# Performance work log

Measured on AMD Instinct MI355X. Metric: run time of the kernel, lower is better.

Reference implementation:

```python
import jax, jax.numpy as jnp
import numpy as np

B, S, H = 1, 2048, 2048
NH, NKV, HD = 16, 4, 128          # heads, kv heads, head_dim
RHD = 64                          # rope head dim
QC, KVC = 1536, 512               # q / kv latent dims
EPS = 1e-6
SCALE = (HD + RHD) ** -0.5


def rms_norm(x, w):
    var = jnp.mean(x.astype(jnp.float32) ** 2, axis=-1, keepdims=True)
    return (x * jax.lax.rsqrt(var + EPS) * w).astype(x.dtype)


def rotate_half(x):
    x1, x2 = x[..., : x.shape[-1] // 2], x[..., x.shape[-1] // 2:]
    return jnp.concatenate([-x2, x1], axis=-1)


def apply_rope(q, k, cos, sin):
    cos = cos[:, None, :, :]  # [B,1,S,RHD]
    sin = sin[:, None, :, :]
    return q * cos + rotate_half(q) * sin, k * cos + rotate_half(k) * sin


def setup_inputs() -> dict:
    key = jax.random.key(0)
    ks = jax.random.split(key, 12)
    X = jax.random.normal(ks[0], (B, S, H), jnp.float32)
    # rotary tables
    inv_freq = 1.0 / (10000.0 ** (np.arange(0, RHD, 2, dtype=np.float32) / RHD))
    t = np.arange(S, dtype=np.float32)
    freqs = np.outer(t, inv_freq)               # [S, RHD/2]
    emb = np.concatenate([freqs, freqs], -1)    # [S, RHD]
    cos = jnp.asarray(np.cos(emb))[None].repeat(B, 0)
    sin = jnp.asarray(np.sin(emb))[None].repeat(B, 0)
    mask = jnp.tril(jnp.ones((S, S), jnp.int32))[None].repeat(B, 0)  # causal
    sc = lambda fan_in: 1.0 / np.sqrt(fan_in)
    return dict(
        X=X, cos=cos, sin=sin, mask=mask,
        w_down_q=jax.random.normal(ks[1], (H, QC), jnp.float32) * sc(H),
        w_up_q=jax.random.normal(ks[2], (QC, H), jnp.float32) * sc(QC),
        w_qr=jax.random.normal(ks[3], (QC, NH * RHD), jnp.float32) * sc(QC),
        w_down_kv=jax.random.normal(ks[4], (H, KVC), jnp.float32) * sc(H),
        w_up_k=jax.random.normal(ks[5], (KVC, NKV * HD), jnp.float32) * sc(KVC),
        w_up_v=jax.random.normal(ks[6], (KVC, NKV * HD), jnp.float32) * sc(KVC),
        w_kr=jax.random.normal(ks[7], (H, RHD), jnp.float32) * sc(H),
        w_o=jax.random.normal(ks[8], (H, H), jnp.float32) * sc(H),
        q_norm_w=jnp.ones((QC,), jnp.float32),
        k_norm_w=jnp.ones((KVC,), jnp.float32),
    )


def reference(X, cos, sin, mask, w_down_q, w_up_q, w_qr, w_down_kv,
              w_up_k, w_up_v, w_kr, w_o, q_norm_w, k_norm_w):
    bsz, q_len, _ = X.shape
    n_rep = NH // NKV
    # --- Q path: down-project, RMSNorm, up-project + rope branch ---
    cq = rms_norm(X @ w_down_q, q_norm_w)                    # [B,S,QC]
    qc = (cq @ w_up_q).reshape(bsz, q_len, NH, HD).transpose(0, 2, 1, 3)
    qr = (cq @ w_qr).reshape(bsz, q_len, NH, RHD).transpose(0, 2, 1, 3)
    # --- KV path ---
    ckv = rms_norm(X @ w_down_kv, k_norm_w)                  # [B,S,KVC]
    kc = (ckv @ w_up_k).reshape(bsz, q_len, NKV, HD).transpose(0, 2, 1, 3)
    kr = (X @ w_kr).reshape(bsz, q_len, 1, RHD).transpose(0, 2, 1, 3)
    kc = jnp.repeat(kc, n_rep, axis=1)                       # [B,NH,S,HD]
    kr = jnp.broadcast_to(kr, (bsz, NH, q_len, RHD))         # repeat_kv(kr, NH)
    qr, kr = apply_rope(qr, kr, cos, sin)
    query = jnp.concatenate([qc, qr], axis=-1)               # [B,NH,S,HD+RHD]
    key = jnp.concatenate([kc, kr], axis=-1)
    value = (ckv @ w_up_v).reshape(bsz, q_len, NKV, HD).transpose(0, 2, 1, 3)
    value = jnp.repeat(value, n_rep, axis=1)                 # [B,NH,S,HD]
    # --- attention ---
    scores = jnp.einsum('bhqd,bhkd->bhqk', query, key) * SCALE
    scores = jnp.where(mask[:, None] == 0, -1e9, scores)
    attn = jax.nn.softmax(scores, axis=-1)                   # dropout p=0
    ctx = jnp.einsum('bhqk,bhkd->bhqd', attn, value)
    ctx = ctx.transpose(0, 2, 1, 3).reshape(bsz, q_len, NH * HD)
    return ctx @ w_o, attn
```

## Files before the change

### kernel.cpp

```cpp
#include <hip/hip_runtime.h>
#include <stdint.h>

typedef __bf16 bf16;
typedef __bf16 bf16x8 __attribute__((ext_vector_type(8)));
typedef __bf16 bf16x4 __attribute__((ext_vector_type(4)));
typedef float f32x4 __attribute__((ext_vector_type(4)));

#define DEVFN static __device__ __forceinline__

constexpr int S = 2048, Hdim = 2048, NH = 16, NKV = 4, HD = 128, RHD = 64, QC = 1536, KVC = 512;
constexpr int QKD = HD + RHD;
constexpr int DN = 2112;
constexpr float RMS_EPS = 1e-6f;
constexpr float ATT_SCALE = 0.07216878364870323f;

DEVFN float wave_sum(float v) {
#pragma unroll
  for (int o = 32; o > 0; o >>= 1) v += __shfl_xor(v, o, 64);
  return v;
}
DEVFN float block_sum(float v) {
  __shared__ float red_s[4];
  v = wave_sum(v);
  int lane = threadIdx.x & 63, wid = threadIdx.x >> 6;
  if (lane == 0) red_s[wid] = v;
  __syncthreads();
  v = red_s[0] + red_s[1] + red_s[2] + red_s[3];
  __syncthreads();
  return v;
}

DEVFN void lgkm_barrier() {
  asm volatile("s_waitcnt lgkmcnt(0)" ::: "memory");
  __builtin_amdgcn_s_barrier();
}

template <typename OT>
DEVFN void gemm_core_pipe(const bf16* __restrict__ A, const bf16* __restrict__ Bt,
                          OT* __restrict__ C, int N, int lda, int ldb, int ldc,
                          int m0, int n0, float scale, int kend) {
  __shared__ alignas(16) bf16 As[2][128 * 32];
  __shared__ alignas(16) bf16 Bs[2][128 * 32];
  const int t = threadIdx.x;
  const int lane = t & 63;
  const int wm = ((t >> 7) & 1) * 64;
  const int wn = ((t >> 6) & 1) * 64;
  const int lr = lane & 15;
  const int lk = (lane >> 4) * 8;
  const int srow = t >> 2;
  const int scol = (t & 3) * 8;
  const bf16* A0 = A + (size_t)(m0 + srow) * lda + scol;
  const bf16* A1 = A + (size_t)(m0 + 64 + srow) * lda + scol;
  const bf16* B0 = Bt + (size_t)(n0 + srow) * ldb + scol;
  const bf16* B1 = Bt + (size_t)(n0 + 64 + srow) * ldb + scol;

  f32x4 acc[4][4];
#pragma unroll
  for (int i = 0; i < 4; i++)
#pragma unroll
    for (int j = 0; j < 4; j++) { f32x4 z = {0.f, 0.f, 0.f, 0.f}; acc[i][j] = z; }

  bf16x8 ca0 = *reinterpret_cast<const bf16x8*>(A0);
  bf16x8 ca1 = *reinterpret_cast<const bf16x8*>(A1);
  bf16x8 cb0 = *reinterpret_cast<const bf16x8*>(B0);
  bf16x8 cb1 = *reinterpret_cast<const bf16x8*>(B1);
  int cur = 0;
  for (int kk = 0; kk < kend; kk += 32) {
    bf16x8 na0, na1, nb0, nb1;
    if (kk + 32 < kend) {
      na0 = *reinterpret_cast<const bf16x8*>(A0 + kk + 32);
      na1 = *reinterpret_cast<const bf16x8*>(A1 + kk + 32);
      nb0 = *reinterpret_cast<const bf16x8*>(B0 + kk + 32);
      nb1 = *reinterpret_cast<const bf16x8*>(B1 + kk + 32);
    }
    *reinterpret_cast<bf16x8*>(&As[cur][t * 8]) = ca0;
    *reinterpret_cast<bf16x8*>(&As[cur][t * 8 + 2048]) = ca1;
    *reinterpret_cast<bf16x8*>(&Bs[cur][t * 8]) = cb0;
    *reinterpret_cast<bf16x8*>(&Bs[cur][t * 8 + 2048]) = cb1;
    lgkm_barrier();
    bf16x8 a[4], b[4];
#pragma unroll
    for (int i = 0; i < 4; i++)
      a[i] = *reinterpret_cast<const bf16x8*>(&As[cur][(wm + i * 16 + lr) * 32 + lk]);
#pragma unroll
    for (int i = 0; i < 4; i++)
      b[i] = *reinterpret_cast<const bf16x8*>(&Bs[cur][(wn + i * 16 + lr) * 32 + lk]);
    __builtin_amdgcn_s_setprio(1);
#pragma unroll
    for (int i = 0; i < 4; i++)
#pragma unroll
      for (int j = 0; j < 4; j++)
        acc[i][j] = __builtin_amdgcn_mfma_f32_16x16x32_bf16(a[i], b[j], acc[i][j], 0, 0, 0);
    __builtin_amdgcn_s_setprio(0);
    ca0 = na0; ca1 = na1; cb0 = nb0; cb1 = nb1;
    cur ^= 1;
  }
  const int orow = (lane >> 4) * 4;
#pragma unroll
  for (int i = 0; i < 4; i++) {
#pragma unroll
    for (int j = 0; j < 4; j++) {
      int col = n0 + wn + j * 16 + lr;
      if (col < N) {
#pragma unroll
        for (int q = 0; q < 4; q++) {
          int row = m0 + wm + i * 16 + orow + q;
          C[(size_t)row * ldc + col] = (OT)(acc[i][j][q] * scale);
        }
      }
    }
  }
}

template <typename OT>
__global__ __launch_bounds__(256) void gemm_nt(const bf16* __restrict__ A, const bf16* __restrict__ Bt,
                                               OT* __restrict__ C, int N, int K, int lda,
                                               int ldb, int ldc, float scale) {
  gemm_core_pipe<OT>(A, Bt, C, N, lda, ldb, ldc, blockIdx.y * 128, blockIdx.x * 128, scale, K);
}

__global__ __launch_bounds__(256) void gemm_up_both(const bf16* __restrict__ cqb,
                                                    const bf16* __restrict__ ckvb,
                                                    const bf16* __restrict__ wt_up1,
                                                    const bf16* __restrict__ wt_up2,
                                                    bf16* __restrict__ up1,
                                                    bf16* __restrict__ up2) {
  int id = blockIdx.x;
  if (id < 384) {
    gemm_core_pipe<bf16>(cqb, wt_up1, up1, 3072, QC, QC, 3072, (id / 24) * 128, (id % 24) * 128, 1.f, QC);
  } else {
    id -= 384;
    gemm_core_pipe<bf16>(ckvb, wt_up2, up2, 1024, KVC, KVC, 1024, (id / 8) * 128, (id % 8) * 128, 1.f, KVC);
  }
}

__global__ __launch_bounds__(512) void fa_fused(const bf16* __restrict__ qpack,
                                                const bf16* __restrict__ kpack,
                                                const bf16* __restrict__ vt,
                                                float* __restrict__ attn,
                                                bf16* __restrict__ ctxb) {
  const int h = blockIdx.y;
  const int g = h >> 2;
  __shared__ alignas(16) bf16 Ks[2][64 * 200];
  __shared__ alignas(16) bf16 Vs[3][128 * 72];
  __shared__ alignas(16) bf16 Ps[3][64 * 72];
  float2* sb = reinterpret_cast<float2*>(&Vs[0][0]);
  float2* statf = sb + 128;

  const int t = threadIdx.x;
  const int lane = t & 63;
  const int w = t >> 6;
  const int wm = (w & 3) * 16;
  const int kh = w >> 2;
  const int lr = lane & 15;
  const int hi = lane >> 4;
  const int lk = hi * 8;
  const int kr0 = t / 24, kc0 = (t % 24) * 8;
  const int kr1 = (t + 512) / 24, kc1 = ((t + 512) % 24) * 8;
  const int kr2 = (t + 1024) / 24, kc2 = ((t + 1024) % 24) * 8;
  const int vr0 = t >> 3, vc0 = (t & 7) * 8;
  const int vr1 = (t + 512) >> 3, vc1 = ((t + 512) & 7) * 8;

  const bf16* Qg = qpack + (size_t)h * S * QKD;
  const bf16* Kg = kpack + (size_t)g * S * QKD;
  const bf16* Vg = vt + (size_t)g * HD * S;
  float* Ah = attn + (size_t)h * S * S;
  bf16* C = ctxb + h * HD;

  for (int sub = 0; sub < 2; ++sub) {
    const int m0 = sub ? (1984 - 64 * blockIdx.x) : (64 * blockIdx.x);
    const int ntiles = sub ? (32 - blockIdx.x) : (blockIdx.x + 1);
    const int kend = m0 + 64;
    __syncthreads();

    bf16x8 qf[6];
#pragma unroll
    for (int ks = 0; ks < 6; ++ks)
      qf[ks] = *reinterpret_cast<const bf16x8*>(&Qg[(size_t)(m0 + wm + lr) * QKD + ks * 32 + lk]);

    float mreg[4] = {-1e30f, -1e30f, -1e30f, -1e30f};
    float lreg[4] = {0.f, 0.f, 0.f, 0.f};
    bf16x8 ck0 = *reinterpret_cast<const bf16x8*>(&Kg[(size_t)kr0 * QKD + kc0]);
    bf16x8 ck1 = *reinterpret_cast<const bf16x8*>(&Kg[(size_t)kr1 * QKD + kc1]);
    bf16x8 ck2 = *reinterpret_cast<const bf16x8*>(&Kg[(size_t)kr2 * QKD + kc2]);
    int cur = 0;
    for (int ti = 0; ti < ntiles; ++ti) {
      const int kt = ti * 64;
      bf16x8 nk0, nk1, nk2;
      if (ti + 1 < ntiles) {
        nk0 = *reinterpret_cast<const bf16x8*>(&Kg[(size_t)(kt + 64 + kr0) * QKD + kc0]);
        nk1 = *reinterpret_cast<const bf16x8*>(&Kg[(size_t)(kt + 64 + kr1) * QKD + kc1]);
        nk2 = *reinterpret_cast<const bf16x8*>(&Kg[(size_t)(kt + 64 + kr2) * QKD + kc2]);
      }
      *reinterpret_cast<bf16x8*>(&Ks[cur][kr0 * 200 + kc0]) = ck0;
      *reinterpret_cast<bf16x8*>(&Ks[cur][kr1 * 200 + kc1]) = ck1;
      *reinterpret_cast<bf16x8*>(&Ks[cur][kr2 * 200 + kc2]) = ck2;
      lgkm_barrier();
      f32x4 acc[2];
#pragma unroll
      for (int kb = 0; kb < 2; kb++) { f32x4 z = {0.f, 0.f, 0.f, 0.f}; acc[kb] = z; }
      __builtin_amdgcn_s_setprio(1);
#pragma unroll
      for (int ks = 0; ks < 6; ++ks) {
#pragma unroll
        for (int kb = 0; kb < 2; ++kb) {
          bf16x8 b = *reinterpret_cast<const bf16x8*>(&Ks[cur][(kh * 32 + kb * 16 + lr) * 200 + ks * 32 + lk]);
          acc[kb] = __builtin_amdgcn_mfma_f32_16x16x32_bf16(qf[ks], b, acc[kb], 0, 0, 0);
        }
      }
      __builtin_amdgcn_s_setprio(0);
      const int colb = kt + kh * 32 + lr;
#pragma unroll
      for (int q = 0; q < 4; ++q) {
        const int rowg = m0 + wm + hi * 4 + q;
        bool u0 = (colb <= rowg), u1 = (colb + 16 <= rowg);
        float s0 = u0 ? acc[0][q] * ATT_SCALE : -1e30f;
        float s1 = u1 ? acc[1][q] * ATT_SCALE : -1e30f;
        float nm = fmaxf(mreg[q], fmaxf(s0, s1));
        float e0 = u0 ? __expf(s0 - nm) : 0.f;
        float e1 = u1 ? __expf(s1 - nm) : 0.f;
        lreg[q] = lreg[q] * __expf(mreg[q] - nm) + e0 + e1;
        mreg[q] = nm;
      }
      ck0 = nk0; ck1 = nk1; ck2 = nk2;
      cur ^= 1;
    }
#pragma unroll
    for (int q = 0; q < 4; ++q) {
      float m = mreg[q], l = lreg[q];
#pragma unroll
      for (int o = 1; o < 16; o <<= 1) {
        float mo = __shfl_xor(m, o, 64);
        float lo = __shfl_xor(l, o, 64);
        float M = fmaxf(m, mo);
        l = l * __expf(m - M) + lo * __expf(mo - M);
        m = M;
      }
      mreg[q] = m; lreg[q] = l;
    }
    __syncthreads();
    if (lr == 0) {
#pragma unroll
      for (int q = 0; q < 4; ++q)
        sb[kh * 64 + wm + hi * 4 + q] = make_float2(mreg[q], lreg[q]);
    }
    __syncthreads();
    if (w < 4 && lr == 0) {
#pragma unroll
      for (int q = 0; q < 4; ++q) {
        int r = wm + hi * 4 + q;
        float2 a = sb[r], b = sb[64 + r];
        float M = fmaxf(a.x, b.x);
        float L = a.y * __expf(a.x - M) + b.y * __expf(b.x - M);
        statf[r] = make_float2(M, 1.0f / L);
      }
    }
    __syncthreads();
    float mr[4], invl[4];
#pragma unroll
    for (int q = 0; q < 4; ++q) {
      float2 sv = statf[wm + hi * 4 + q];
      mr[q] = sv.x; invl[q] = sv.y;
    }
    __syncthreads();

    f32x4 accp[4];
#pragma unroll
    for (int j = 0; j < 4; j++) { f32x4 z = {0.f, 0.f, 0.f, 0.f}; accp[j] = z; }
    ck0 = *reinterpret_cast<const bf16x8*>(&Kg[(size_t)kr0 * QKD + kc0]);
    ck1 = *reinterpret_cast<const bf16x8*>(&Kg[(size_t)kr1 * QKD + kc1]);
    ck2 = *reinterpret_cast<const bf16x8*>(&Kg[(size_t)kr2 * QKD + kc2]);
    bf16x8 cv0 = *reinterpret_cast<const bf16x8*>(&Vg[(size_t)vr0 * S + vc0]);
    bf16x8 cv1 = *reinterpret_cast<const bf16x8*>(&Vg[(size_t)vr1 * S + vc1]);
    cur = 0;
    int pb = 0;
    for (int ti = 0; ti < ntiles; ++ti) {
      const int kt = ti * 64;
      bf16x8 nk0, nk1, nk2, nv0, nv1;
      if (ti + 1 < ntiles) {
        nk0 = *reinterpret_cast<const bf16x8*>(&Kg[(size_t)(kt + 64 + kr0) * QKD + kc0]);
        nk1 = *reinterpret_cast<const bf16x8*>(&Kg[(size_t)(kt + 64 + kr1) * QKD + kc1]);
        nk2 = *reinterpret_cast<const bf16x8*>(&Kg[(size_t)(kt + 64 + kr2) * QKD + kc2]);
        nv0 = *reinterpret_cast<const bf16x8*>(&Vg[(size_t)vr0 * S + kt + 64 + vc0]);
        nv1 = *reinterpret_cast<const bf16x8*>(&Vg[(size_t)vr1 * S + kt + 64 + vc1]);
      }
      *reinterpret_cast<bf16x8*>(&Ks[cur][kr0 * 200 + kc0]) = ck0;
      *reinterpret_cast<bf16x8*>(&Ks[cur][kr1 * 200 + kc1]) = ck1;
      *reinterpret_cast<bf16x8*>(&Ks[cur][kr2 * 200 + kc2]) = ck2;
      *reinterpret_cast<bf16x8*>(&Vs[pb][vr0 * 72 + vc0]) = cv0;
      *reinterpret_cast<bf16x8*>(&Vs[pb][vr1 * 72 + vc1]) = cv1;
      lgkm_barrier();
      f32x4 acc[2];
#pragma unroll
      for (int kb = 0; kb < 2; kb++) { f32x4 z = {0.f, 0.f, 0.f, 0.f}; acc[kb] = z; }
      __builtin_amdgcn_s_setprio(1);
#pragma unroll
      for (int ks = 0; ks < 6; ++ks) {
#pragma unroll
        for (int kb = 0; kb < 2; ++kb) {
          bf16x8 b = *reinterpret_cast<const bf16x8*>(&Ks[cur][(kh * 32 + kb * 16 + lr) * 200 + ks * 32 + lk]);
          acc[kb] = __builtin_amdgcn_mfma_f32_16x16x32_bf16(qf[ks], b, acc[kb], 0, 0, 0);
        }
      }
      __builtin_amdgcn_s_setprio(0);
      const int colb = kt + kh * 32 + lr;
#pragma unroll
      for (int kb = 0; kb < 2; ++kb) {
#pragma unroll
        for (int q = 0; q < 4; ++q) {
          const int rloc = wm + hi * 4 + q;
          const int rowg = m0 + rloc;
          const int col = colb + kb * 16;
          float s = acc[kb][q] * ATT_SCALE;
          float p = (col <= rowg) ? __expf(s - mr[q]) * invl[q] : 0.f;
          Ah[(size_t)rowg * S + col] = p;
          Ps[pb][rloc * 72 + kh * 32 + kb * 16 + lr] = (bf16)p;
        }
      }
      if (ti > 0) {
        const int pp = (pb == 0) ? 2 : pb - 1;
        __builtin_amdgcn_s_setprio(1);
#pragma unroll
        for (int ks = 0; ks < 2; ++ks) {
          bf16x8 a = *reinterpret_cast<const bf16x8*>(&Ps[pp][(wm + lr) * 72 + ks * 32 + lk]);
#pragma unroll
          for (int j = 0; j < 4; ++j) {
            bf16x8 b = *reinterpret_cast<const bf16x8*>(&Vs[pp][(kh * 64 + j * 16 + lr) * 72 + ks * 32 + lk]);
            accp[j] = __builtin_amdgcn_mfma_f32_16x16x32_bf16(a, b, accp[j], 0, 0, 0);
          }
        }
        __builtin_amdgcn_s_setprio(0);
      }
      ck0 = nk0; ck1 = nk1; ck2 = nk2; cv0 = nv0; cv1 = nv1;
      cur ^= 1;
      pb = (pb == 2) ? 0 : pb + 1;
    }
    lgkm_barrier();
    {
      const int pp = (pb == 0) ? 2 : pb - 1;
#pragma unroll
      for (int ks = 0; ks < 2; ++ks) {
        bf16x8 a = *reinterpret_cast<const bf16x8*>(&Ps[pp][(wm + lr) * 72 + ks * 32 + lk]);
#pragma unroll
        for (int j = 0; j < 4; ++j) {
          bf16x8 b = *reinterpret_cast<const bf16x8*>(&Vs[pp][(kh * 64 + j * 16 + lr) * 72 + ks * 32 + lk]);
          accp[j] = __builtin_amdgcn_mfma_f32_16x16x32_bf16(a, b, accp[j], 0, 0, 0);
        }
      }
    }

    const float4 zz = make_float4(0.f, 0.f, 0.f, 0.f);
    {
      const int zr = t >> 3, zc0 = (t & 7) * 4;
      float* zrow = Ah + (size_t)(m0 + zr) * S;
      for (int k = kend + zc0; k < S; k += 32) *reinterpret_cast<float4*>(zrow + k) = zz;
    }

#pragma unroll
    for (int j = 0; j < 4; ++j) {
      const int d = kh * 64 + j * 16 + lr;
#pragma unroll
      for (int q = 0; q < 4; ++q) {
        const int rowg = m0 + wm + hi * 4 + q;
        C[(size_t)rowg * Hdim + d] = (bf16)accp[j][q];
      }
    }
  }
}

struct TJobs {
  const float* src[8];
  bf16* dst[8];
  int R[8], C[8], tiles[8];
};

__global__ __launch_bounds__(256) void prep(const float* __restrict__ Xf,
                                            bf16* __restrict__ Xb, TJobs J) {
  const int t = threadIdx.x;
  int id = blockIdx.x;
  if (id < 2048) {
    size_t i = (size_t)id * 256 + t;
    float4 f0 = *reinterpret_cast<const float4*>(Xf + i * 8);
    float4 f1 = *reinterpret_cast<const float4*>(Xf + i * 8 + 4);
    bf16x8 v;
    v[0] = (bf16)f0.x; v[1] = (bf16)f0.y; v[2] = (bf16)f0.z; v[3] = (bf16)f0.w;
    v[4] = (bf16)f1.x; v[5] = (bf16)f1.y; v[6] = (bf16)f1.z; v[7] = (bf16)f1.w;
    *reinterpret_cast<bf16x8*>(Xb + i * 8) = v;
    return;
  }
  int tile = id - 2048;
  int j = 0;
  while (tile >= J.tiles[j]) { tile -= J.tiles[j]; ++j; }
  const int C = J.C[j], R = J.R[j];
  int tcn = C >> 5;
  int rb = (tile / tcn) * 32, cb = (tile % tcn) * 32;
  const float* in = J.src[j];
  bf16* out = J.dst[j];
  __shared__ float tl[32][33];
  int tx = t & 31, ty = t >> 5;
#pragma unroll
  for (int q = 0; q < 32; q += 8)
    tl[ty + q][tx] = in[(size_t)(rb + ty + q) * C + cb + tx];
  __syncthreads();
#pragma unroll
  for (int q = 0; q < 32; q += 8)
    out[(size_t)(cb + ty + q) * R + rb + tx] = (bf16)tl[tx][ty + q];
}

__global__ __launch_bounds__(256) void rmsnorm_fused(const float* __restrict__ dproj,
                                                     const float* __restrict__ qw,
                                                     const float* __restrict__ kw,
                                                     bf16* __restrict__ cqb,
                                                     bf16* __restrict__ ckvb) {
  int row = blockIdx.x;
  bool isq = (blockIdx.y == 0);
  int C = isq ? QC : KVC;
  const float* p = dproj + (size_t)row * DN + (isq ? 0 : QC);
  const float* w = isq ? qw : kw;
  bf16* out = (isq ? cqb : ckvb) + (size_t)row * C;
  float ss = 0.f;
  for (int i = threadIdx.x * 4; i < C; i += 1024) {
    float4 v = *reinterpret_cast<const float4*>(p + i);
    ss += v.x * v.x + v.y * v.y + v.z * v.z + v.w * v.w;
  }
  ss = block_sum(ss);
  float r = rsqrtf(ss / (float)C + RMS_EPS);
  for (int i = threadIdx.x * 4; i < C; i += 1024) {
    float4 v = *reinterpret_cast<const float4*>(p + i);
    float4 g = *reinterpret_cast<const float4*>(w + i);
    bf16x4 o;
    o[0] = (bf16)(v.x * r * g.x); o[1] = (bf16)(v.y * r * g.y);
    o[2] = (bf16)(v.z * r * g.z); o[3] = (bf16)(v.w * r * g.w);
    *reinterpret_cast<bf16x4*>(out + i) = o;
  }
}

__global__ __launch_bounds__(256) void pack_all(const bf16* __restrict__ up1,
                                                const bf16* __restrict__ up2,
                                                const float* __restrict__ dproj,
                                                const float* __restrict__ cosp,
                                                const float* __restrict__ sinp,
                                                bf16* __restrict__ qpack,
                                                bf16* __restrict__ kpack,
                                                bf16* __restrict__ vt) {
  const int t = threadIdx.x;
  int id = blockIdx.x;
  if (id < 3072) {
    int idx = id * 256 + t;
    const int P = NH * S * 16;
    if (idx < P) {
      int d8 = idx & 15, s = (idx >> 4) & (S - 1), h = idx >> 15;
      int4 v = *reinterpret_cast<const int4*>(up1 + (size_t)s * 3072 + h * HD + d8 * 8);
      *reinterpret_cast<int4*>(qpack + ((size_t)h * S + s) * QKD + d8 * 8) = v;
    } else {
      int j = idx - P;
      int d0 = (j & 7) * 8, s = (j >> 3) & (S - 1), h = j >> 14;
      const bf16* xr = up1 + (size_t)s * 3072 + 2048 + h * RHD;
      bf16x8 xa = *reinterpret_cast<const bf16x8*>(xr + d0);
      bf16x8 xb = *reinterpret_cast<const bf16x8*>(xr + (d0 ^ 32));
      float sign = (d0 < 32) ? -1.f : 1.f;
      const float* cr = cosp + s * RHD + d0;
      const float* sr = sinp + s * RHD + d0;
      bf16x8 o;
#pragma unroll
      for (int i = 0; i < 8; i++)
        o[i] = (bf16)((float)xa[i] * cr[i] + sign * (float)xb[i] * sr[i]);
      *reinterpret_cast<bf16x8*>(qpack + ((size_t)h * S + s) * QKD + HD + d0) = o;
    }
    return;
  }
  if (id < 3648) {
    int idx = (id - 3072) * 256 + t;
    const int P = NKV * S * 16;
    if (idx < P) {
      int d8 = idx & 15, s = (idx >> 4) & (S - 1), g = idx >> 15;
      int4 v = *reinterpret_cast<const int4*>(up2 + (size_t)s * 1024 + g * HD + d8 * 8);
      *reinterpret_cast<int4*>(kpack + ((size_t)g * S + s) * QKD + d8 * 8) = v;
    } else {
      int j = idx - P;
      int d0 = (j & 7) * 8, s = j >> 3;
      const float* xr = dproj + (size_t)s * DN + 2048;
      float4 a0 = *reinterpret_cast<const float4*>(xr + d0);
      float4 a1 = *reinterpret_cast<const float4*>(xr + d0 + 4);
      float4 b0 = *reinterpret_cast<const float4*>(xr + (d0 ^ 32));
      float4 b1 = *reinterpret_cast<const float4*>(xr + (d0 ^ 32) + 4);
      float sign = (d0 < 32) ? -1.f : 1.f;
      const float* cr = cosp + s * RHD + d0;
      const float* sr = sinp + s * RHD + d0;
      float xa[8] = {a0.x, a0.y, a0.z, a0.w, a1.x, a1.y, a1.z, a1.w};
      float xb[8] = {b0.x, b0.y, b0.z, b0.w, b1.x, b1.y, b1.z, b1.w};
      bf16x8 o;
#pragma unroll
      for (int i = 0; i < 8; i++)
        o[i] = (bf16)(xa[i] * cr[i] + sign * xb[i] * sr[i]);
#pragma unroll
      for (int g = 0; g < NKV; g++)
        *reinterpret_cast<bf16x8*>(kpack + ((size_t)g * S + s) * QKD + HD + d0) = o;
    }
    return;
  }
  int tile = id - 3648;
  int cb = (tile & 15) * 32;
  int rb = (tile >> 4) * 32;
  __shared__ float tl[32][33];
  int tx = t & 31, ty = t >> 5;
  const bf16* in = up2 + 512;
#pragma unroll
  for (int q = 0; q < 32; q += 8)
    tl[ty + q][tx] = (float)in[(size_t)(rb + ty + q) * 1024 + cb + tx];
  __syncthreads();
#pragma unroll
  for (int q = 0; q < 32; q += 8)
    vt[(size_t)(cb + ty + q) * S + rb + tx] = (bf16)tl[tx][ty + q];
}

extern "C" void kernel_launch(void* const* d_in, const int* in_sizes, int n_in, void* d_out,
                              int out_size, void* d_ws, size_t ws_size, hipStream_t stream) {
  const float* Xf = (const float*)d_in[0];
  const float* cosp = (const float*)d_in[1];
  const float* sinp = (const float*)d_in[2];
  const float* w_down_q = (const float*)d_in[4];
  const float* w_up_q = (const float*)d_in[5];
  const float* w_qr = (const float*)d_in[6];
  const float* w_down_kv = (const float*)d_in[7];
  const float* w_up_k = (const float*)d_in[8];
  const float* w_up_v = (const float*)d_in[9];
  const float* w_kr = (const float*)d_in[10];
  const float* w_o = (const float*)d_in[11];
  const float* q_norm_w = (const float*)d_in[12];
  const float* k_norm_w = (const float*)d_in[13];

  float* out0 = (float*)d_out;
  float* attn = out0 + (size_t)S * Hdim;

  char* base = (char*)d_ws;
  size_t off = 0;
  auto carve = [&](size_t bytes) -> void* {
    void* p = base + off;
    off += (bytes + 255) & ~(size_t)255;
    return p;
  };
  bf16* Xb      = (bf16*)carve((size_t)S * Hdim * 2);
  bf16* wt_down = (bf16*)carve((size_t)2176 * 2048 * 2);
  bf16* wt_up1  = (bf16*)carve((size_t)3072 * QC * 2);
  bf16* wt_up2  = (bf16*)carve((size_t)1024 * KVC * 2);
  bf16* wt_o    = (bf16*)carve((size_t)Hdim * Hdim * 2);
  float* dproj  = (float*)carve((size_t)S * DN * 4);
  bf16* cqb     = (bf16*)carve((size_t)S * QC * 2);
  bf16* ckvb    = (bf16*)carve((size_t)S * KVC * 2);
  bf16* up1     = (bf16*)carve((size_t)S * 3072 * 2);
  bf16* up2     = (bf16*)carve((size_t)S * 1024 * 2);
  bf16* qpack   = (bf16*)carve((size_t)NH * S * QKD * 2);
  bf16* kpack   = (bf16*)carve((size_t)NKV * S * QKD * 2);
  bf16* vt      = (bf16*)carve((size_t)NKV * HD * S * 2);
  bf16* ctxb    = (bf16*)carve((size_t)S * Hdim * 2);
  (void)in_sizes; (void)n_in; (void)out_size; (void)ws_size;

  TJobs J;
  const float* srcs[8] = {w_down_q, w_down_kv, w_kr, w_up_q, w_qr, w_up_k, w_up_v, w_o};
  bf16* dsts[8] = {wt_down, wt_down + (size_t)QC * 2048, wt_down + (size_t)2048 * 2048,
                   wt_up1, wt_up1 + (size_t)2048 * QC, wt_up2, wt_up2 + (size_t)512 * KVC, wt_o};
  int Rs[8] = {2048, 2048, 2048, 1536, 1536, 512, 512, 2048};
  int Cs[8] = {1536, 512, 64, 2048, 1024, 512, 512, 2048};
  int total_tiles = 0;
  for (int j = 0; j < 8; j++) {
    J.src[j] = srcs[j]; J.dst[j] = dsts[j]; J.R[j] = Rs[j]; J.C[j] = Cs[j];
    J.tiles[j] = (Rs[j] / 32) * (Cs[j] / 32);
    total_tiles += J.tiles[j];
  }

  prep<<<2048 + total_tiles, 256, 0, stream>>>(Xf, Xb, J);
  gemm_nt<float><<<dim3(17, 16), 256, 0, stream>>>(Xb, wt_down, dproj, DN, Hdim, Hdim, Hdim, DN, 1.f);
  rmsnorm_fused<<<dim3(S, 2), 256, 0, stream>>>(dproj, q_norm_w, k_norm_w, cqb, ckvb);
  gemm_up_both<<<512, 256, 0, stream>>>(cqb, ckvb, wt_up1, wt_up2, up1, up2);
  pack_all<<<4672, 256, 0, stream>>>(up1, up2, dproj, cosp, sinp, qpack, kpack, vt);
  fa_fused<<<dim3(16, NH), 512, 0, stream>>>(qpack, kpack, vt, attn, ctxb);
  gemm_nt<float><<<dim3(16, 16), 256, 0, stream>>>(ctxb, wt_o, out0, Hdim, Hdim, Hdim, Hdim, Hdim, 1.f);
}
```

Baseline: 306.8 us.

## Split fused attention into stats and PV kernels with key-range halves

The fused attention kernel becomes two kernels, each launched with twice the blocks: every block handles one half of the key tiles. The first kernel writes partial row max and sum statistics to global memory. The second merges the two halves' statistics, writes the probabilities, and accumulates partial context in fp32 over 32-wide key tiles. A third kernel adds the two partial contexts and converts the sum to bf16. The aim is more parallelism and occupancy than the previous 256-block grid, at the cost of extra launches, fp32 partial-context traffic, and a second read of Q and K.

Result: slower. 346.5 us (+12.9%).

```diff
diff --git a/kernel.cpp b/kernel.cpp
--- a/kernel.cpp
+++ b/kernel.cpp
@@ -134,18 +134,13 @@
   }
 }
 
-__global__ __launch_bounds__(512) void fa_fused(const bf16* __restrict__ qpack,
-                                                const bf16* __restrict__ kpack,
-                                                const bf16* __restrict__ vt,
-                                                float* __restrict__ attn,
-                                                bf16* __restrict__ ctxb) {
-  const int h = blockIdx.y;
+__global__ __launch_bounds__(512, 4) void fa_stats(const bf16* __restrict__ qpack,
+                                                   const bf16* __restrict__ kpack,
+                                                   float* __restrict__ stats2) {
+  const int ib = blockIdx.x, half = blockIdx.y, h = blockIdx.z;
   const int g = h >> 2;
   __shared__ alignas(16) bf16 Ks[2][64 * 200];
-  __shared__ alignas(16) bf16 Vs[3][128 * 72];
-  __shared__ alignas(16) bf16 Ps[3][64 * 72];
-  float2* sb = reinterpret_cast<float2*>(&Vs[0][0]);
-  float2* statf = sb + 128;
+  __shared__ float2 sb[128];
 
   const int t = threadIdx.x;
   const int lane = t & 63;
@@ -158,19 +153,15 @@
   const int kr0 = t / 24, kc0 = (t % 24) * 8;
   const int kr1 = (t + 512) / 24, kc1 = ((t + 512) % 24) * 8;
   const int kr2 = (t + 1024) / 24, kc2 = ((t + 1024) % 24) * 8;
-  const int vr0 = t >> 3, vc0 = (t & 7) * 8;
-  const int vr1 = (t + 512) >> 3, vc1 = ((t + 512) & 7) * 8;
-
   const bf16* Qg = qpack + (size_t)h * S * QKD;
   const bf16* Kg = kpack + (size_t)g * S * QKD;
-  const bf16* Vg = vt + (size_t)g * HD * S;
-  float* Ah = attn + (size_t)h * S * S;
-  bf16* C = ctxb + h * HD;
 
   for (int sub = 0; sub < 2; ++sub) {
-    const int m0 = sub ? (1984 - 64 * blockIdx.x) : (64 * blockIdx.x);
-    const int ntiles = sub ? (32 - blockIdx.x) : (blockIdx.x + 1);
-    const int kend = m0 + 64;
+    const int m0 = sub ? (1984 - 64 * ib) : (64 * ib);
+    const int ntF = sub ? (32 - ib) : (ib + 1);
+    const int n0 = (ntF + 1) >> 1;
+    const int t0 = half ? n0 : 0;
+    const int t1 = half ? ntF : n0;
     __syncthreads();
 
     bf16x8 qf[6];
@@ -180,50 +171,52 @@
 
     float mreg[4] = {-1e30f, -1e30f, -1e30f, -1e30f};
     float lreg[4] = {0.f, 0.f, 0.f, 0.f};
-    bf16x8 ck0 = *reinterpret_cast<const bf16x8*>(&Kg[(size_t)kr0 * QKD + kc0]);
-    bf16x8 ck1 = *reinterpret_cast<const bf16x8*>(&Kg[(size_t)kr1 * QKD + kc1]);
-    bf16x8 ck2 = *reinterpret_cast<const bf16x8*>(&Kg[(size_t)kr2 * QKD + kc2]);
-    int cur = 0;
-    for (int ti = 0; ti < ntiles; ++ti) {
-      const int kt = ti * 64;
-      bf16x8 nk0, nk1, nk2;
-      if (ti + 1 < ntiles) {
-        nk0 = *reinterpret_cast<const bf16x8*>(&Kg[(size_t)(kt + 64 + kr0) * QKD + kc0]);
-        nk1 = *reinterpret_cast<const bf16x8*>(&Kg[(size_t)(kt + 64 + kr1) * QKD + kc1]);
-        nk2 = *reinterpret_cast<const bf16x8*>(&Kg[(size_t)(kt + 64 + kr2) * QKD + kc2]);
-      }
-      *reinterpret_cast<bf16x8*>(&Ks[cur][kr0 * 200 + kc0]) = ck0;
-      *reinterpret_cast<bf16x8*>(&Ks[cur][kr1 * 200 + kc1]) = ck1;
-      *reinterpret_cast<bf16x8*>(&Ks[cur][kr2 * 200 + kc2]) = ck2;
-      lgkm_barrier();
-      f32x4 acc[2];
-#pragma unroll
-      for (int kb = 0; kb < 2; kb++) { f32x4 z = {0.f, 0.f, 0.f, 0.f}; acc[kb] = z; }
-      __builtin_amdgcn_s_setprio(1);
-#pragma unroll
-      for (int ks = 0; ks < 6; ++ks) {
-#pragma unroll
-        for (int kb = 0; kb < 2; ++kb) {
-          bf16x8 b = *reinterpret_cast<const bf16x8*>(&Ks[cur][(kh * 32 + kb * 16 + lr) * 200 + ks * 32 + lk]);
-          acc[kb] = __builtin_amdgcn_mfma_f32_16x16x32_bf16(qf[ks], b, acc[kb], 0, 0, 0);
+    if (t0 < t1) {
+      bf16x8 ck0 = *reinterpret_cast<const bf16x8*>(&Kg[(size_t)(t0 * 64 + kr0) * QKD + kc0]);
+      bf16x8 ck1 = *reinterpret_cast<const bf16x8*>(&Kg[(size_t)(t0 * 64 + kr1) * QKD + kc1]);
+      bf16x8 ck2 = *reinterpret_cast<const bf16x8*>(&Kg[(size_t)(t0 * 64 + kr2) * QKD + kc2]);
+      int cur = 0;
+      for (int ti = t0; ti < t1; ++ti) {
+        const int kt = ti * 64;
+        bf16x8 nk0, nk1, nk2;
+        if (ti + 1 < t1) {
+          nk0 = *reinterpret_cast<const bf16x8*>(&Kg[(size_t)(kt + 64 + kr0) * QKD + kc0]);
+          nk1 = *reinterpret_cast<const bf16x8*>(&Kg[(size_t)(kt + 64 + kr1) * QKD + kc1]);
+          nk2 = *reinterpret_cast<const bf16x8*>(&Kg[(size_t)(kt + 64 + kr2) * QKD + kc2]);
         }
-      }
-      __builtin_amdgcn_s_setprio(0);
-      const int colb = kt + kh * 32 + lr;
-#pragma unroll
-      for (int q = 0; q < 4; ++q) {
-        const int rowg = m0 + wm + hi * 4 + q;
-        bool u0 = (colb <= rowg), u1 = (colb + 16 <= rowg);
-        float s0 = u0 ? acc[0][q] * ATT_SCALE : -1e30f;
-        float s1 = u1 ? acc[1][q] * ATT_SCALE : -1e30f;
-        float nm = fmaxf(mreg[q], fmaxf(s0, s1));
-        float e0 = u0 ? __expf(s0 - nm) : 0.f;
-        float e1 = u1 ? __expf(s1 - nm) : 0.f;
-        lreg[q] = lreg[q] * __expf(mreg[q] - nm) + e0 + e1;
-        mreg[q] = nm;
-      }
-      ck0 = nk0; ck1 = nk1; ck2 = nk2;
-      cur ^= 1;
+        *reinterpret_cast<bf16x8*>(&Ks[cur][kr0 * 200 + kc0]) = ck0;
+        *reinterpret_cast<bf16x8*>(&Ks[cur][kr1 * 200 + kc1]) = ck1;
+        *reinterpret_cast<bf16x8*>(&Ks[cur][kr2 * 200 + kc2]) = ck2;
+        lgkm_barrier();
+        f32x4 acc[2];
+#pragma unroll
+        for (int kb = 0; kb < 2; kb++) { f32x4 z = {0.f, 0.f, 0.f, 0.f}; acc[kb] = z; }
+        __builtin_amdgcn_s_setprio(1);
+#pragma unroll
+        for (int ks = 0; ks < 6; ++ks) {
+#pragma unroll
+          for (int kb = 0; kb < 2; ++kb) {
+            bf16x8 b = *reinterpret_cast<const bf16x8*>(&Ks[cur][(kh * 32 + kb * 16 + lr) * 200 + ks * 32 + lk]);
+            acc[kb] = __builtin_amdgcn_mfma_f32_16x16x32_bf16(qf[ks], b, acc[kb], 0, 0, 0);
+          }
+        }
+        __builtin_amdgcn_s_setprio(0);
+        const int colb = kt + kh * 32 + lr;
+#pragma unroll
+        for (int q = 0; q < 4; ++q) {
+          const int rowg = m0 + wm + hi * 4 + q;
+          bool u0 = (colb <= rowg), u1 = (colb + 16 <= rowg);
+          float s0 = u0 ? acc[0][q] * ATT_SCALE : -1e30f;
+          float s1 = u1 ? acc[1][q] * ATT_SCALE : -1e30f;
+          float nm = fmaxf(mreg[q], fmaxf(s0, s1));
+          float e0 = u0 ? __expf(s0 - nm) : 0.f;
+          float e1 = u1 ? __expf(s1 - nm) : 0.f;
+          lreg[q] = lreg[q] * __expf(mreg[q] - nm) + e0 + e1;
+          mreg[q] = nm;
+        }
+        ck0 = nk0; ck1 = nk1; ck2 = nk2;
+        cur ^= 1;
+      }
     }
 #pragma unroll
     for (int q = 0; q < 4; ++q) {
@@ -252,105 +245,135 @@
         float2 a = sb[r], b = sb[64 + r];
         float M = fmaxf(a.x, b.x);
         float L = a.y * __expf(a.x - M) + b.y * __expf(b.x - M);
-        statf[r] = make_float2(M, 1.0f / L);
-      }
-    }
+        stats2[(((size_t)half * NH + h) * S + m0 + r) * 2] = M;
+        stats2[(((size_t)half * NH + h) * S + m0 + r) * 2 + 1] = L;
+      }
+    }
+  }
+}
+
+__global__ __launch_bounds__(512, 4) void fa_pv(const bf16* __restrict__ qpack,
+                                                const bf16* __restrict__ kpack,
+                                                const bf16* __restrict__ vt,
+                                                const float* __restrict__ stats2,
+                                                float* __restrict__ attn,
+                                                float* __restrict__ octxA,
+                                                float* __restrict__ octxB) {
+  const int ib = blockIdx.x, half = blockIdx.y, h = blockIdx.z;
+  const int g = h >> 2;
+  __shared__ alignas(16) bf16 Ks[2][32 * 200];
+  __shared__ alignas(16) bf16 Vs[3][128 * 40];
+  __shared__ alignas(16) bf16 Ps[3][64 * 40];
+
+  const int t = threadIdx.x;
+  const int lane = t & 63;
+  const int w = t >> 6;
+  const int wm = (w & 3) * 16;
+  const int kh = w >> 2;
+  const int lr = lane & 15;
+  const int hi = lane >> 4;
+  const int lk = hi * 8;
+  const int kr0 = t / 24, kc0 = (t % 24) * 8;
+  const int kr1 = (t + 512) / 24, kc1 = ((t + 512) % 24) * 8;
+  const int vr0 = t >> 2, vc0 = (t & 3) * 8;
+
+  const bf16* Qg = qpack + (size_t)h * S * QKD;
+  const bf16* Kg = kpack + (size_t)g * S * QKD;
+  const bf16* Vg = vt + (size_t)g * HD * S;
+  float* Ah = attn + (size_t)h * S * S;
+  float* octx = half ? octxB : octxA;
+
+  for (int sub = 0; sub < 2; ++sub) {
+    const int m0 = sub ? (1984 - 64 * ib) : (64 * ib);
+    const int ntF = sub ? (64 - 2 * ib) : (2 * ib + 2);
+    const int nh = ntF >> 1;
+    const int t0 = half * nh, t1 = t0 + nh;
+    const int kend = m0 + 64;
     __syncthreads();
+
+    bf16x8 qf[6];
+#pragma unroll
+    for (int ks = 0; ks < 6; ++ks)
+      qf[ks] = *reinterpret_cast<const bf16x8*>(&Qg[(size_t)(m0 + wm + lr) * QKD + ks * 32 + lk]);
+
     float mr[4], invl[4];
 #pragma unroll
     for (int q = 0; q < 4; ++q) {
-      float2 sv = statf[wm + hi * 4 + q];
-      mr[q] = sv.x; invl[q] = sv.y;
-    }
-    __syncthreads();
+      const size_t rowg = (size_t)m0 + wm + hi * 4 + q;
+      float2 a = *reinterpret_cast<const float2*>(&stats2[((size_t)h * S + rowg) * 2]);
+      float2 b = *reinterpret_cast<const float2*>(&stats2[(((size_t)NH + h) * S + rowg) * 2]);
+      float M = fmaxf(a.x, b.x);
+      float L = a.y * __expf(a.x - M) + b.y * __expf(b.x - M);
+      mr[q] = M; invl[q] = 1.0f / L;
+    }
 
     f32x4 accp[4];
 #pragma unroll
     for (int j = 0; j < 4; j++) { f32x4 z = {0.f, 0.f, 0.f, 0.f}; accp[j] = z; }
-    ck0 = *reinterpret_cast<const bf16x8*>(&Kg[(size_t)kr0 * QKD + kc0]);
-    ck1 = *reinterpret_cast<const bf16x8*>(&Kg[(size_t)kr1 * QKD + kc1]);
-    ck2 = *reinterpret_cast<const bf16x8*>(&Kg[(size_t)kr2 * QKD + kc2]);
-    bf16x8 cv0 = *reinterpret_cast<const bf16x8*>(&Vg[(size_t)vr0 * S + vc0]);
-    bf16x8 cv1 = *reinterpret_cast<const bf16x8*>(&Vg[(size_t)vr1 * S + vc1]);
-    cur = 0;
-    int pb = 0;
-    for (int ti = 0; ti < ntiles; ++ti) {
-      const int kt = ti * 64;
-      bf16x8 nk0, nk1, nk2, nv0, nv1;
-      if (ti + 1 < ntiles) {
-        nk0 = *reinterpret_cast<const bf16x8*>(&Kg[(size_t)(kt + 64 + kr0) * QKD + kc0]);
-        nk1 = *reinterpret_cast<const bf16x8*>(&Kg[(size_t)(kt + 64 + kr1) * QKD + kc1]);
-        nk2 = *reinterpret_cast<const bf16x8*>(&Kg[(size_t)(kt + 64 + kr2) * QKD + kc2]);
-        nv0 = *reinterpret_cast<const bf16x8*>(&Vg[(size_t)vr0 * S + kt + 64 + vc0]);
-        nv1 = *reinterpret_cast<const bf16x8*>(&Vg[(size_t)vr1 * S + kt + 64 + vc1]);
+
+    bf16x8 ck0 = *reinterpret_cast<const bf16x8*>(&Kg[(size_t)(t0 * 32 + kr0) * QKD + kc0]);
+    bf16x8 ck1 = *reinterpret_cast<const bf16x8*>(&Kg[(size_t)(t0 * 32 + kr1) * QKD + kc1]);
+    bf16x8 cv0 = *reinterpret_cast<const bf16x8*>(&Vg[(size_t)vr0 * S + t0 * 32 + vc0]);
+    int cur = 0, pb = 0;
+    for (int ti = t0; ti < t1; ++ti) {
+      const int kt = ti * 32;
+      bf16x8 nk0, nk1, nv0;
+      if (ti + 1 < t1) {
+        nk0 = *reinterpret_cast<const bf16x8*>(&Kg[(size_t)(kt + 32 + kr0) * QKD + kc0]);
+        nk1 = *reinterpret_cast<const bf16x8*>(&Kg[(size_t)(kt + 32 + kr1) * QKD + kc1]);
+        nv0 = *reinterpret_cast<const bf16x8*>(&Vg[(size_t)vr0 * S + kt + 32 + vc0]);
       }
       *reinterpret_cast<bf16x8*>(&Ks[cur][kr0 * 200 + kc0]) = ck0;
-      *reinterpret_cast<bf16x8*>(&Ks[cur][kr1 * 200 + kc1]) = ck1;
-      *reinterpret_cast<bf16x8*>(&Ks[cur][kr2 * 200 + kc2]) = ck2;
-      *reinterpret_cast<bf16x8*>(&Vs[pb][vr0 * 72 + vc0]) = cv0;
-      *reinterpret_cast<bf16x8*>(&Vs[pb][vr1 * 72 + vc1]) = cv1;
+      if (t < 256)
+        *reinterpret_cast<bf16x8*>(&Ks[cur][kr1 * 200 + kc1]) = ck1;
+      *reinterpret_cast<bf16x8*>(&Vs[pb][vr0 * 40 + vc0]) = cv0;
       lgkm_barrier();
-      f32x4 acc[2];
-#pragma unroll
-      for (int kb = 0; kb < 2; kb++) { f32x4 z = {0.f, 0.f, 0.f, 0.f}; acc[kb] = z; }
+      f32x4 acc = {0.f, 0.f, 0.f, 0.f};
       __builtin_amdgcn_s_setprio(1);
 #pragma unroll
       for (int ks = 0; ks < 6; ++ks) {
-#pragma unroll
-        for (int kb = 0; kb < 2; ++kb) {
-          bf16x8 b = *reinterpret_cast<const bf16x8*>(&Ks[cur][(kh * 32 + kb * 16 + lr) * 200 + ks * 32 + lk]);
-          acc[kb] = __builtin_amdgcn_mfma_f32_16x16x32_bf16(qf[ks], b, acc[kb], 0, 0, 0);
-        }
+        bf16x8 b = *reinterpret_cast<const bf16x8*>(&Ks[cur][(kh * 16 + lr) * 200 + ks * 32 + lk]);
+        acc = __builtin_amdgcn_mfma_f32_16x16x32_bf16(qf[ks], b, acc, 0, 0, 0);
       }
       __builtin_amdgcn_s_setprio(0);
-      const int colb = kt + kh * 32 + lr;
-#pragma unroll
-      for (int kb = 0; kb < 2; ++kb) {
-#pragma unroll
-        for (int q = 0; q < 4; ++q) {
-          const int rloc = wm + hi * 4 + q;
-          const int rowg = m0 + rloc;
-          const int col = colb + kb * 16;
-          float s = acc[kb][q] * ATT_SCALE;
-          float p = (col <= rowg) ? __expf(s - mr[q]) * invl[q] : 0.f;
-          Ah[(size_t)rowg * S + col] = p;
-          Ps[pb][rloc * 72 + kh * 32 + kb * 16 + lr] = (bf16)p;
-        }
-      }
-      if (ti > 0) {
+      const int col = kt + kh * 16 + lr;
+#pragma unroll
+      for (int q = 0; q < 4; ++q) {
+        const int rloc = wm + hi * 4 + q;
+        const int rowg = m0 + rloc;
+        float s = acc[q] * ATT_SCALE;
+        float p = (col <= rowg) ? __expf(s - mr[q]) * invl[q] : 0.f;
+        Ah[(size_t)rowg * S + col] = p;
+        Ps[pb][rloc * 40 + kh * 16 + lr] = (bf16)p;
+      }
+      if (ti > t0) {
         const int pp = (pb == 0) ? 2 : pb - 1;
         __builtin_amdgcn_s_setprio(1);
-#pragma unroll
-        for (int ks = 0; ks < 2; ++ks) {
-          bf16x8 a = *reinterpret_cast<const bf16x8*>(&Ps[pp][(wm + lr) * 72 + ks * 32 + lk]);
-#pragma unroll
-          for (int j = 0; j < 4; ++j) {
-            bf16x8 b = *reinterpret_cast<const bf16x8*>(&Vs[pp][(kh * 64 + j * 16 + lr) * 72 + ks * 32 + lk]);
-            accp[j] = __builtin_amdgcn_mfma_f32_16x16x32_bf16(a, b, accp[j], 0, 0, 0);
-          }
+        bf16x8 a = *reinterpret_cast<const bf16x8*>(&Ps[pp][(wm + lr) * 40 + lk]);
+#pragma unroll
+        for (int j = 0; j < 4; ++j) {
+          bf16x8 b = *reinterpret_cast<const bf16x8*>(&Vs[pp][(kh * 64 + j * 16 + lr) * 40 + lk]);
+          accp[j] = __builtin_amdgcn_mfma_f32_16x16x32_bf16(a, b, accp[j], 0, 0, 0);
         }
         __builtin_amdgcn_s_setprio(0);
       }
-      ck0 = nk0; ck1 = nk1; ck2 = nk2; cv0 = nv0; cv1 = nv1;
+      ck0 = nk0; ck1 = nk1; cv0 = nv0;
       cur ^= 1;
       pb = (pb == 2) ? 0 : pb + 1;
     }
     lgkm_barrier();
     {
       const int pp = (pb == 0) ? 2 : pb - 1;
-#pragma unroll
-      for (int ks = 0; ks < 2; ++ks) {
-        bf16x8 a = *reinterpret_cast<const bf16x8*>(&Ps[pp][(wm + lr) * 72 + ks * 32 + lk]);
-#pragma unroll
-        for (int j = 0; j < 4; ++j) {
-          bf16x8 b = *reinterpret_cast<const bf16x8*>(&Vs[pp][(kh * 64 + j * 16 + lr) * 72 + ks * 32 + lk]);
-          accp[j] = __builtin_amdgcn_mfma_f32_16x16x32_bf16(a, b, accp[j], 0, 0, 0);
-        }
-      }
-    }
-
-    const float4 zz = make_float4(0.f, 0.f, 0.f, 0.f);
-    {
+      bf16x8 a = *reinterpret_cast<const bf16x8*>(&Ps[pp][(wm + lr) * 40 + lk]);
+#pragma unroll
+      for (int j = 0; j < 4; ++j) {
+        bf16x8 b = *reinterpret_cast<const bf16x8*>(&Vs[pp][(kh * 64 + j * 16 + lr) * 40 + lk]);
+        accp[j] = __builtin_amdgcn_mfma_f32_16x16x32_bf16(a, b, accp[j], 0, 0, 0);
+      }
+    }
+
+    if (half == 1) {
+      const float4 zz = make_float4(0.f, 0.f, 0.f, 0.f);
       const int zr = t >> 3, zc0 = (t & 7) * 4;
       float* zrow = Ah + (size_t)(m0 + zr) * S;
       for (int k = kend + zc0; k < S; k += 32) *reinterpret_cast<float4*>(zrow + k) = zz;
@@ -362,10 +385,26 @@
 #pragma unroll
       for (int q = 0; q < 4; ++q) {
         const int rowg = m0 + wm + hi * 4 + q;
-        C[(size_t)rowg * Hdim + d] = (bf16)accp[j][q];
-      }
-    }
-  }
+        octx[(size_t)rowg * Hdim + h * HD + d] = accp[j][q];
+      }
+    }
+  }
+}
+
+__global__ __launch_bounds__(256) void combine_ctx(const float* __restrict__ a,
+                                                   const float* __restrict__ b,
+                                                   bf16* __restrict__ ctxb) {
+  size_t i = ((size_t)blockIdx.x * 256 + threadIdx.x) * 8;
+  float4 a0 = *reinterpret_cast<const float4*>(a + i);
+  float4 a1 = *reinterpret_cast<const float4*>(a + i + 4);
+  float4 b0 = *reinterpret_cast<const float4*>(b + i);
+  float4 b1 = *reinterpret_cast<const float4*>(b + i + 4);
+  bf16x8 o;
+  o[0] = (bf16)(a0.x + b0.x); o[1] = (bf16)(a0.y + b0.y);
+  o[2] = (bf16)(a0.z + b0.z); o[3] = (bf16)(a0.w + b0.w);
+  o[4] = (bf16)(a1.x + b1.x); o[5] = (bf16)(a1.y + b1.y);
+  o[6] = (bf16)(a1.z + b1.z); o[7] = (bf16)(a1.w + b1.w);
+  *reinterpret_cast<bf16x8*>(ctxb + i) = o;
 }
 
 struct TJobs {
@@ -554,6 +593,9 @@
   bf16* kpack   = (bf16*)carve((size_t)NKV * S * QKD * 2);
   bf16* vt      = (bf16*)carve((size_t)NKV * HD * S * 2);
   bf16* ctxb    = (bf16*)carve((size_t)S * Hdim * 2);
+  float* stats2 = (float*)carve((size_t)2 * NH * S * 2 * 4);
+  float* octxA  = (float*)carve((size_t)S * Hdim * 4);
+  float* octxB  = (float*)carve((size_t)S * Hdim * 4);
   (void)in_sizes; (void)n_in; (void)out_size; (void)ws_size;
 
   TJobs J;
@@ -574,6 +616,8 @@
   rmsnorm_fused<<<dim3(S, 2), 256, 0, stream>>>(dproj, q_norm_w, k_norm_w, cqb, ckvb);
   gemm_up_both<<<512, 256, 0, stream>>>(cqb, ckvb, wt_up1, wt_up2, up1, up2);
   pack_all<<<4672, 256, 0, stream>>>(up1, up2, dproj, cosp, sinp, qpack, kpack, vt);
-  fa_fused<<<dim3(16, NH), 512, 0, stream>>>(qpack, kpack, vt, attn, ctxb);
+  fa_stats<<<dim3(16, 2, NH), 512, 0, stream>>>(qpack, kpack, stats2);
+  fa_pv<<<dim3(16, 2, NH), 512, 0, stream>>>(qpack, kpack, vt, stats2, attn, octxA, octxB);
+  combine_ctx<<<S * Hdim / 8 / 256, 256, 0, stream>>>(octxA, octxB, ctxb);
   gemm_nt<float><<<dim3(16, 16), 256, 0, stream>>>(ctxb, wt_o, out0, Hdim, Hdim, Hdim, Hdim, Hdim, 1.f);
 }
```
